# Performance work log

Measured on AMD Instinct MI355X. Metric: run time of the kernel, lower is better.

The kernel has to match this reference:

```python
import jax, jax.numpy as jnp
import numpy as np

B = 1024      # batch
H = 512       # n_hidden
F = 32        # lstm_features
CIN = 4       # input channels
K = 30        # conv kernel
STRIDE = 6
L = 924       # input length -> T = (924-30)//6+1 = 150
KD = 40       # deconv kernel
NSTEPS = 10   # lstm_future_out
DN = ('NCH', 'OIH', 'NCH')


def setup_inputs() -> dict:
    key = jax.random.key(0)
    ks = jax.random.split(key, 14)
    s = 0.05
    rn = lambda k, shape: jax.random.normal(k, shape, jnp.float32) * s
    return dict(
        x=jax.random.normal(ks[0], (B, CIN, L), jnp.float32),
        conv_w=rn(ks[1], (F, CIN, K)), conv_b=rn(ks[2], (F,)),
        Wih0=rn(ks[3], (4 * H, F)), Whh0=rn(ks[4], (4 * H, H)),
        bih0=rn(ks[5], (4 * H,)), bhh0=rn(ks[6], (4 * H,)),
        Wih1=rn(ks[7], (4 * H, H)), Whh1=rn(ks[8], (4 * H, H)),
        bih1=rn(ks[9], (4 * H,)), bhh1=rn(ks[10], (4 * H,)),
        dec_w=rn(ks[11], (F, H)), dec_b=rn(ks[12], (F,)),
        deconv_w=rn(ks[13], (F, 1, KD)),
    )


def _cell(x, h, c, Wih, Whh, b):
    # PyTorch LSTM gate order: i, f, g, o
    g = x @ Wih.T + h @ Whh.T + b
    i, f, gg, o = jnp.split(g, 4, axis=-1)
    c = jax.nn.sigmoid(f) * c + jax.nn.sigmoid(i) * jnp.tanh(gg)
    h = jax.nn.sigmoid(o) * jnp.tanh(c)
    return h, c


def _lstm_layer(seq, Wih, Whh, b):
    # seq: [T, B, in] -> ys: [T, B, H], final (h, c)
    n = seq.shape[1]
    h0 = jnp.zeros((n, H), seq.dtype)
    c0 = jnp.zeros((n, H), seq.dtype)
    def step(carry, x):
        h, c = _cell(x, carry[0], carry[1], Wih, Whh, b)
        return (h, c), h
    (hT, cT), ys = jax.lax.scan(step, (h0, c0), seq)
    return ys, hT, cT


def _forward(x, conv_w, conv_b, Wih0, Whh0, bih0, bhh0,
             Wih1, Whh1, bih1, bhh1, dec_w, dec_b, deconv_w):
    # encoder conv: [B,4,L] -> [B,F,T]
    z = jax.lax.conv_general_dilated(x, conv_w, (STRIDE,), [(0, 0)],
                                     dimension_numbers=DN) + conv_b[None, :, None]
    z = jax.nn.relu(z)
    seq = jnp.transpose(z, (2, 0, 1))  # [T, B, F]
    b0, b1 = bih0 + bhh0, bih1 + bhh1
    s0, h0, c0 = _lstm_layer(seq, Wih0, Whh0, b0)
    s1, h1, c1 = _lstm_layer(s0, Wih1, Whh1, b1)
    out = s1 @ dec_w.T + dec_b                 # [T, B, F]
    y0 = out[-1]                               # output[-2:-1] of encoder -> last decoded step
    def dec_step(carry, _):
        y, ha, ca, hb, cb = carry
        ha, ca = _cell(y, ha, ca, Wih0, Whh0, b0)
        hb, cb = _cell(ha, hb, cb, Wih1, Whh1, b1)
        y = hb @ dec_w.T + dec_b
        return (y, ha, ca, hb, cb), y
    _, fut = jax.lax.scan(dec_step, (y0, h0, c0, h1, c1), None, length=NSTEPS)
    fut = jnp.transpose(fut, (1, 2, 0))        # [B, F, 10]
    # ConvTranspose1d (stride=1, pad=0, no bias) == cross-correlation with
    # spatially flipped, channel-swapped kernel on input padded by KD-1.
    kt = jnp.transpose(jnp.flip(deconv_w, -1), (1, 0, 2))  # [1, F, KD]
    return jax.lax.conv_general_dilated(fut, kt, (1,), [(KD - 1, KD - 1)],
                                        dimension_numbers=DN)  # [B, 1, 49]


def reference(x, conv_w, conv_b, Wih0, Whh0, bih0, bhh0,
              Wih1, Whh1, bih1, bhh1, dec_w, dec_b, deconv_w):
    return _forward(x, conv_w, conv_b, Wih0, Whh0, bih0, bhh0,
                    Wih1, Whh1, bih1, bhh1, dec_w, dec_b, deconv_w)
```

## Files before the change

kernel.cpp:

```cpp
#include <hip/hip_runtime.h>
#include <hip/hip_bf16.h>

typedef __hip_bfloat16 bf16;
typedef __attribute__((ext_vector_type(8))) short short8;
typedef __attribute__((ext_vector_type(4))) float float4v;

#define B_    1024
#define H_    512
#define G4H   2048
#define F_    32
#define CIN_  4
#define K_    30
#define STRIDE_ 6
#define L_    924
#define T_    150
#define KD_   40
#define NSTEPS_ 10
#define BH    (B_ * H_)
#define STRF  16

__device__ __forceinline__ float sigmoidf_(float x) { return 1.f / (1.f + __expf(-x)); }
__device__ __forceinline__ float tanhf_(float x)    { return 1.f - 2.f / (__expf(2.f * x) + 1.f); }
__device__ __forceinline__ float b2f_(short s) {
    return __uint_as_float(((unsigned)(unsigned short)s) << 16);
}
__device__ __forceinline__ void stwt_(bf16* p, float v) {
    union { __hip_bfloat16 b; unsigned short u; } cv;
    cv.b = __float2bfloat16(v);
    __hip_atomic_store((unsigned short*)p, cv.u, __ATOMIC_RELAXED, __HIP_MEMORY_SCOPE_AGENT);
}

__global__ __launch_bounds__(256) void cvt_kernel(const float* __restrict__ src,
                                                  bf16* __restrict__ dst, int n) {
    int i = blockIdx.x * 256 + threadIdx.x;
    if (i < n) dst[i] = __float2bfloat16(src[i]);
}

__global__ void bias_kernel(const float* __restrict__ bih0, const float* __restrict__ bhh0,
                            const float* __restrict__ bih1, const float* __restrict__ bhh1,
                            float* __restrict__ b0, float* __restrict__ b1) {
    int i = blockIdx.x * 256 + threadIdx.x;
    if (i < G4H)      b0[i] = bih0[i] + bhh0[i];
    else if (i < 2*G4H) { int j = i - G4H; b1[j] = bih1[j] + bhh1[j]; }
}

__global__ __launch_bounds__(256) void conv_kernel(
    const float* __restrict__ x, const float* __restrict__ w,
    const float* __restrict__ cb, bf16* __restrict__ seq)
{
    __shared__ float w_lds[CIN_ * K_ * F_];
    __shared__ float x_lds[CIN_ * L_];
    int tid = threadIdx.x;
    int b = blockIdx.x;
    for (int i = tid; i < CIN_ * K_ * F_; i += 256) {
        int f = i & 31, r = i >> 5;
        w_lds[r * 32 + f] = w[f * (CIN_ * K_) + r];
    }
    const float* xb = x + (size_t)b * (CIN_ * L_);
    for (int i = tid; i < CIN_ * L_; i += 256)
        x_lds[i] = xb[i];
    __syncthreads();
    int f = tid & 31, tt = tid >> 5;
    float cbf = cb[f];
    for (int t0 = 0; t0 < T_; t0 += 8) {
        int t = t0 + tt;
        if (t < T_) {
            float acc = cbf;
            #pragma unroll
            for (int c = 0; c < CIN_; ++c) {
                const float* xr = x_lds + c * L_ + t * STRIDE_;
                const float* wr = w_lds + c * K_ * 32 + f;
                #pragma unroll
                for (int k = 0; k < K_; ++k)
                    acc += xr[k] * wr[k * 32];
            }
            acc = fmaxf(acc, 0.f);
            seq[(size_t)t * (B_ * F_) + b * F_ + f] = __float2bfloat16(acc);
        }
    }
}

__device__ __forceinline__ void wait2(const int* fa, int ta, const int* fb, int tb) {
    const int t = threadIdx.x;
    if (t < 64) {
        const int* p = nullptr; int tgt = 0;
        if (t < 32) { if (fa) { p = fa + t * STRF;        tgt = ta; } }
        else        { if (fb) { p = fb + (t - 32) * STRF; tgt = tb; } }
        for (;;) {
            int v = p ? __hip_atomic_load(p, __ATOMIC_RELAXED, __HIP_MEMORY_SCOPE_AGENT)
                      : 0x7fffffff;
            if (__all(v >= tgt)) break;
            __builtin_amdgcn_s_sleep(2);
        }
    }
    __syncthreads();
    __builtin_amdgcn_fence(__ATOMIC_ACQUIRE, "agent");
}

__device__ __forceinline__ void signal1(int* f, int val) {
    __syncthreads();
    if (threadIdx.x == 0) {
        __builtin_amdgcn_s_waitcnt(0);
        __hip_atomic_store(f, val, __ATOMIC_RELAXED, __HIP_MEMORY_SCOPE_AGENT);
    }
}

template<int P1KS, int XSTR>
__device__ __forceinline__ void layer_step(
    const bf16* __restrict__ X, const bf16* __restrict__ Hprev,
    const short8* __restrict__ WldsH, const short8* __restrict__ WldsI,
    const float* __restrict__ bias, float (&creg)[16], bf16* __restrict__ Hout,
    int m0, int j0, int wid, int lane)
{
    const int row16 = lane & 15;
    const int quad  = lane >> 4;
    const int mrow  = m0 + wid * 64 + row16;

    float4v acc[4][4];
    #pragma unroll
    for (int ms = 0; ms < 4; ++ms)
        #pragma unroll
        for (int g = 0; g < 4; ++g)
            acc[ms][g] = (float4v){0.f, 0.f, 0.f, 0.f};

    for (int ks = 0; ks < P1KS; ++ks) {
        short8 av[4];
        #pragma unroll
        for (int ms = 0; ms < 4; ++ms)
            av[ms] = *(const short8*)(X + (size_t)(mrow + ms * 16) * XSTR
                                      + ks * 32 + quad * 8);
        #pragma unroll
        for (int g = 0; g < 4; ++g) {
            short8 bfr = WldsI[(ks * 4 + g) * 64 + lane];
            #pragma unroll
            for (int ms = 0; ms < 4; ++ms)
                acc[ms][g] = __builtin_amdgcn_mfma_f32_16x16x32_bf16(av[ms], bfr, acc[ms][g], 0, 0, 0);
        }
    }

    for (int ks = 0; ks < 16; ++ks) {
        short8 av[4];
        #pragma unroll
        for (int ms = 0; ms < 4; ++ms)
            av[ms] = *(const short8*)(Hprev + (size_t)(mrow + ms * 16) * H_
                                      + ks * 32 + quad * 8);
        #pragma unroll
        for (int g = 0; g < 4; ++g) {
            short8 bfr = WldsH[(ks * 4 + g) * 64 + lane];
            #pragma unroll
            for (int ms = 0; ms < 4; ++ms)
                acc[ms][g] = __builtin_amdgcn_mfma_f32_16x16x32_bf16(av[ms], bfr, acc[ms][g], 0, 0, 0);
        }
    }

    const int j = j0 + row16;
    const float bi  = bias[j];
    const float bff = bias[H_ + j];
    const float bg  = bias[2 * H_ + j];
    const float bo  = bias[3 * H_ + j];
    #pragma unroll
    for (int ms = 0; ms < 4; ++ms) {
        #pragma unroll
        for (int r = 0; r < 4; ++r) {
            int brow = m0 + wid * 64 + ms * 16 + quad * 4 + r;
            float ig = sigmoidf_(acc[ms][0][r] + bi);
            float fg = sigmoidf_(acc[ms][1][r] + bff);
            float gg = tanhf_(acc[ms][2][r] + bg);
            float og = sigmoidf_(acc[ms][3][r] + bo);
            float cn = fg * creg[ms * 4 + r] + ig * gg;
            creg[ms * 4 + r] = cn;
            stwt_(Hout + (size_t)brow * H_ + j, og * tanhf_(cn));
        }
    }
}

struct PP {
    const bf16 *seq, *Wih0, *Whh0, *Wih1, *Whh1, *dwb;
    const float *b0, *b1, *dec_b;
    float *fut;
    bf16 *h0, *h1, *y;
    int *flags;
};

__global__ __launch_bounds__(256, 1) void lstm_persist(PP P) {
    __shared__ short8 WldsH[4096];
    __shared__ short8 WldsI[4096];

    const int bid   = blockIdx.x;
    const int gsw   = bid & 7;
    const bool isL0 = (gsw < 4);
    const int mg    = gsw & 3;
    const int jj    = bid >> 3;
    const int lb    = mg * 32 + jj;
    const int j0    = jj * 16;
    const int m0    = mg * 256;
    const int tid   = threadIdx.x;
    const int wid   = tid >> 6;
    const int lane  = tid & 63;

    {
        const bf16* Whh = isL0 ? P.Whh0 : P.Whh1;
        for (int i = 0; i < 16; ++i) {
            int s = tid + i * 256;
            int frag = s >> 6, ln = s & 63;
            int ks = frag >> 2, g = frag & 3;
            WldsH[s] = *(const short8*)(Whh + (size_t)(g * H_ + j0 + (ln & 15)) * H_
                                        + ks * 32 + (ln >> 4) * 8);
        }
        if (isL0) {
            if (tid < 256) {
                int frag = tid >> 6, ln = tid & 63;
                int g = frag & 3;
                WldsI[tid] = *(const short8*)(P.Wih0 + (size_t)(g * H_ + j0 + (ln & 15)) * F_
                                              + (ln >> 4) * 8);
            }
        } else {
            for (int i = 0; i < 16; ++i) {
                int s = tid + i * 256;
                int frag = s >> 6, ln = s & 63;
                int ks = frag >> 2, g = frag & 3;
                WldsI[s] = *(const short8*)(P.Wih1 + (size_t)(g * H_ + j0 + (ln & 15)) * H_
                                            + ks * 32 + (ln >> 4) * 8);
            }
        }
        __syncthreads();
    }

    float creg[16];
    #pragma unroll
    for (int i = 0; i < 16; ++i) creg[i] = 0.f;

    int* f0 = P.flags;
    int* f1 = P.flags + 128 * STRF;
    int* fy = P.flags + 256 * STRF;
    const int* f0g = f0 + mg * 32 * STRF;
    const int* f1g = f1 + mg * 32 * STRF;
    const int* fyg = fy + mg * 32 * STRF;

    if (isL0) {
        for (int t = 0; t < T_; ++t) {
            wait2(f0g, t, f1g, t - 2);
            layer_step<1, 32>(P.seq + (size_t)t * B_ * F_,
                              P.h0 + (size_t)((t + 2) % 3) * BH, WldsH, WldsI, P.b0,
                              creg, P.h0 + (size_t)(t % 3) * BH, m0, j0, wid, lane);
            signal1(f0 + lb * STRF, t + 1);
        }
        for (int s = 0; s <= NSTEPS_; ++s) {
            wait2(f1g, T_ + s, (s >= 1) ? f0g : nullptr, T_ + s);
            {
                int id = lb * 256 + tid;
                int br = id >> 5, f = id & 31;
                const short8* hv = (const short8*)(P.h1 + (size_t)((T_ - 1 + s) % 3) * BH
                                                   + (size_t)br * H_);
                const short8* wv = (const short8*)(P.dwb + (size_t)f * H_);
                float acc = P.dec_b[f];
                for (int i = 0; i < H_ / 8; ++i) {
                    short8 h8 = hv[i], w8 = wv[i];
                    #pragma unroll
                    for (int k = 0; k < 8; ++k)
                        acc += b2f_(h8[k]) * b2f_(w8[k]);
                }
                stwt_(P.y + id, acc);
                if (s >= 1)
                    P.fut[(size_t)br * (F_ * NSTEPS_) + f * NSTEPS_ + (s - 1)] = acc;
            }
            signal1(fy + lb * STRF, s + 1);
            if (s < NSTEPS_) {
                int t = T_ + s;
                wait2(f0g, t, f1g, t - 2);
                wait2(fyg, s + 1, nullptr, 0);
                layer_step<1, 32>(P.y,
                                  P.h0 + (size_t)((t + 2) % 3) * BH, WldsH, WldsI, P.b0,
                                  creg, P.h0 + (size_t)(t % 3) * BH, m0, j0, wid, lane);
                signal1(f0 + lb * STRF, t + 1);
            }
        }
    } else {
        for (int t = 0; t < T_ + NSTEPS_; ++t) {
            wait2(f0g, t + 1, f1g, t);
            layer_step<16, 512>(P.h0 + (size_t)(t % 3) * BH,
                                P.h1 + (size_t)((t + 2) % 3) * BH, WldsH, WldsI, P.b1,
                                creg, P.h1 + (size_t)(t % 3) * BH, m0, j0, wid, lane);
            signal1(f1 + lb * STRF, t + 1);
        }
    }
}

__global__ __launch_bounds__(256) void deconv_kernel(
    const float* __restrict__ fut, const float* __restrict__ dw,
    float* __restrict__ out)
{
    int idx = blockIdx.x * 256 + threadIdx.x;
    if (idx >= B_ * 49) return;
    int b = idx / 49, jj = idx % 49;
    int tlo = jj - (KD_ - 1); if (tlo < 0) tlo = 0;
    int thi = jj; if (thi > NSTEPS_ - 1) thi = NSTEPS_ - 1;
    float acc = 0.f;
    for (int f = 0; f < F_; ++f) {
        const float* fr = fut + (size_t)b * (F_ * NSTEPS_) + f * NSTEPS_;
        const float* wr = dw + f * KD_;
        for (int t = tlo; t <= thi; ++t)
            acc += fr[t] * wr[jj - t];
    }
    out[idx] = acc;
}

extern "C" void kernel_launch(void* const* d_in, const int* in_sizes, int n_in,
                              void* d_out, int out_size, void* d_ws, size_t ws_size,
                              hipStream_t stream) {
    const float* x       = (const float*)d_in[0];
    const float* conv_w  = (const float*)d_in[1];
    const float* conv_b  = (const float*)d_in[2];
    const float* Wih0f   = (const float*)d_in[3];
    const float* Whh0f   = (const float*)d_in[4];
    const float* bih0    = (const float*)d_in[5];
    const float* bhh0    = (const float*)d_in[6];
    const float* Wih1f   = (const float*)d_in[7];
    const float* Whh1f   = (const float*)d_in[8];
    const float* bih1    = (const float*)d_in[9];
    const float* bhh1    = (const float*)d_in[10];
    const float* dec_wf  = (const float*)d_in[11];
    const float* dec_b   = (const float*)d_in[12];
    const float* deconvw = (const float*)d_in[13];
    float* out = (float*)d_out;

    char* ws = (char*)d_ws;
    size_t off = 0;
    auto alloc = [&](size_t bytes) { char* p = ws + off; off = (off + bytes + 255) & ~(size_t)255; return p; };
    bf16*  seq   = (bf16*) alloc((size_t)T_ * B_ * F_ * 2);
    float* b0v   = (float*)alloc(G4H * 4);
    float* b1v   = (float*)alloc(G4H * 4);
    bf16*  h0    = (bf16*) alloc((size_t)3 * BH * 2);
    bf16*  h1    = (bf16*) alloc((size_t)3 * BH * 2);
    bf16*  y     = (bf16*) alloc((size_t)B_ * F_ * 2);
    float* fut   = (float*)alloc((size_t)B_ * F_ * NSTEPS_ * 4);
    bf16*  Wih0b = (bf16*) alloc((size_t)G4H * F_ * 2);
    bf16*  Whh0b = (bf16*) alloc((size_t)G4H * H_ * 2);
    bf16*  Wih1b = (bf16*) alloc((size_t)G4H * H_ * 2);
    bf16*  Whh1b = (bf16*) alloc((size_t)G4H * H_ * 2);
    bf16*  dec_wb= (bf16*) alloc((size_t)F_ * H_ * 2);
    int*   flags = (int*)  alloc(3 * 128 * STRF * 4);

    hipMemsetAsync(h0, 0, (size_t)3 * BH * 2, stream);
    hipMemsetAsync(h1, 0, (size_t)3 * BH * 2, stream);
    hipMemsetAsync(flags, 0, 3 * 128 * STRF * 4, stream);

    cvt_kernel<<<(G4H * F_ + 255) / 256, 256, 0, stream>>>(Wih0f, Wih0b, G4H * F_);
    cvt_kernel<<<(G4H * H_ + 255) / 256, 256, 0, stream>>>(Whh0f, Whh0b, G4H * H_);
    cvt_kernel<<<(G4H * H_ + 255) / 256, 256, 0, stream>>>(Wih1f, Wih1b, G4H * H_);
    cvt_kernel<<<(G4H * H_ + 255) / 256, 256, 0, stream>>>(Whh1f, Whh1b, G4H * H_);
    cvt_kernel<<<(F_ * H_ + 255) / 256, 256, 0, stream>>>(dec_wf, dec_wb, F_ * H_);

    bias_kernel<<<16, 256, 0, stream>>>(bih0, bhh0, bih1, bhh1, b0v, b1v);
    conv_kernel<<<B_, 256, 0, stream>>>(x, conv_w, conv_b, seq);

    PP P;
    P.seq = seq; P.Wih0 = Wih0b; P.Whh0 = Whh0b; P.Wih1 = Wih1b; P.Whh1 = Whh1b;
    P.dwb = dec_wb; P.b0 = b0v; P.b1 = b1v; P.dec_b = dec_b;
    P.fut = fut; P.h0 = h0; P.h1 = h1; P.y = y;
    P.flags = flags;

    void* args[] = { &P };
    hipError_t err = hipLaunchCooperativeKernel((const void*)lstm_persist,
                                                dim3(256), dim3(256), args, 0, stream);
    if (err != hipSuccess) {
        lstm_persist<<<256, 256, 0, stream>>>(P);
    }

    deconv_kernel<<<196, 256, 0, stream>>>(fut, deconvw, out);
}
```

Baseline: 4.870 ms.

## Split LSTM step waits so independent GEMM halves overlap flag polling

```diff
diff --git a/kernel.cpp b/kernel.cpp
--- a/kernel.cpp
+++ b/kernel.cpp
@@ -17,7 +17,6 @@
 #define KD_   40
 #define NSTEPS_ 10
 #define BH    (B_ * H_)
-#define STRF  16
 
 __device__ __forceinline__ float sigmoidf_(float x) { return 1.f / (1.f + __expf(-x)); }
 __device__ __forceinline__ float tanhf_(float x)    { return 1.f - 2.f / (__expf(2.f * x) + 1.f); }
@@ -80,21 +79,23 @@
     }
 }
 
-__device__ __forceinline__ void wait2(const int* fa, int ta, const int* fb, int tb) {
-    const int t = threadIdx.x;
-    if (t < 64) {
-        const int* p = nullptr; int tgt = 0;
-        if (t < 32) { if (fa) { p = fa + t * STRF;        tgt = ta; } }
-        else        { if (fb) { p = fb + (t - 32) * STRF; tgt = tb; } }
-        for (;;) {
-            int v = p ? __hip_atomic_load(p, __ATOMIC_RELAXED, __HIP_MEMORY_SCOPE_AGENT)
-                      : 0x7fffffff;
-            if (__all(v >= tgt)) break;
-            __builtin_amdgcn_s_sleep(2);
-        }
-    }
-    __syncthreads();
-    __builtin_amdgcn_fence(__ATOMIC_ACQUIRE, "agent");
+__device__ __forceinline__ void wait1(const int* fg, int tgt, bool inv) {
+    if (tgt > 0) {
+        if (threadIdx.x < 16) {
+            const long long* p = (const long long*)fg + threadIdx.x;
+            for (int n = 0; ; ++n) {
+                long long v = __hip_atomic_load(p, __ATOMIC_RELAXED, __HIP_MEMORY_SCOPE_AGENT);
+                int a = (int)v, b = (int)(v >> 32);
+                if (__all(a >= tgt && b >= tgt)) break;
+                if (n < 2) __builtin_amdgcn_s_sleep(2);
+                else       __builtin_amdgcn_s_sleep(32);
+            }
+        }
+        __syncthreads();
+        if (inv) __builtin_amdgcn_fence(__ATOMIC_ACQUIRE, "agent");
+    } else {
+        __syncthreads();
+    }
 }
 
 __device__ __forceinline__ void signal1(int* f, int val) {
@@ -105,25 +106,13 @@
     }
 }
 
-template<int P1KS, int XSTR>
-__device__ __forceinline__ void layer_step(
-    const bf16* __restrict__ X, const bf16* __restrict__ Hprev,
-    const short8* __restrict__ WldsH, const short8* __restrict__ WldsI,
-    const float* __restrict__ bias, float (&creg)[16], bf16* __restrict__ Hout,
-    int m0, int j0, int wid, int lane)
+#define MFMA_ __builtin_amdgcn_mfma_f32_16x16x32_bf16
+template<int NKS, int XSTR>
+__device__ __forceinline__ void gemm_acc(
+    const bf16* __restrict__ X, const short8* __restrict__ W,
+    float4v (&acc)[4][4], int mrow, int quad, int lane)
 {
-    const int row16 = lane & 15;
-    const int quad  = lane >> 4;
-    const int mrow  = m0 + wid * 64 + row16;
-
-    float4v acc[4][4];
-    #pragma unroll
-    for (int ms = 0; ms < 4; ++ms)
-        #pragma unroll
-        for (int g = 0; g < 4; ++g)
-            acc[ms][g] = (float4v){0.f, 0.f, 0.f, 0.f};
-
-    for (int ks = 0; ks < P1KS; ++ks) {
+    for (int ks = 0; ks < NKS; ++ks) {
         short8 av[4];
         #pragma unroll
         for (int ms = 0; ms < 4; ++ms)
@@ -131,28 +120,20 @@
                                       + ks * 32 + quad * 8);
         #pragma unroll
         for (int g = 0; g < 4; ++g) {
-            short8 bfr = WldsI[(ks * 4 + g) * 64 + lane];
+            short8 bfr = W[(ks * 4 + g) * 64 + lane];
             #pragma unroll
             for (int ms = 0; ms < 4; ++ms)
-                acc[ms][g] = __builtin_amdgcn_mfma_f32_16x16x32_bf16(av[ms], bfr, acc[ms][g], 0, 0, 0);
-        }
-    }
-
-    for (int ks = 0; ks < 16; ++ks) {
-        short8 av[4];
-        #pragma unroll
-        for (int ms = 0; ms < 4; ++ms)
-            av[ms] = *(const short8*)(Hprev + (size_t)(mrow + ms * 16) * H_
-                                      + ks * 32 + quad * 8);
-        #pragma unroll
-        for (int g = 0; g < 4; ++g) {
-            short8 bfr = WldsH[(ks * 4 + g) * 64 + lane];
-            #pragma unroll
-            for (int ms = 0; ms < 4; ++ms)
-                acc[ms][g] = __builtin_amdgcn_mfma_f32_16x16x32_bf16(av[ms], bfr, acc[ms][g], 0, 0, 0);
-        }
-    }
-
+                acc[ms][g] = MFMA_(av[ms], bfr, acc[ms][g], 0, 0, 0);
+        }
+    }
+}
+
+__device__ __forceinline__ void epilogue_(
+    float4v (&acc)[4][4], float (&creg)[16], const float* __restrict__ bias,
+    bf16* __restrict__ Hout, int m0, int j0, int wid, int lane)
+{
+    const int row16 = lane & 15;
+    const int quad  = lane >> 4;
     const int j = j0 + row16;
     const float bi  = bias[j];
     const float bff = bias[H_ + j];
@@ -197,6 +178,8 @@
     const int tid   = threadIdx.x;
     const int wid   = tid >> 6;
     const int lane  = tid & 63;
+    const int quad  = lane >> 4;
+    const int mrow  = m0 + wid * 64 + (lane & 15);
 
     {
         const bf16* Whh = isL0 ? P.Whh0 : P.Whh1;
@@ -231,57 +214,77 @@
     for (int i = 0; i < 16; ++i) creg[i] = 0.f;
 
     int* f0 = P.flags;
-    int* f1 = P.flags + 128 * STRF;
-    int* fy = P.flags + 256 * STRF;
-    const int* f0g = f0 + mg * 32 * STRF;
-    const int* f1g = f1 + mg * 32 * STRF;
-    const int* fyg = fy + mg * 32 * STRF;
+    int* f1 = P.flags + 128;
+    int* fy = P.flags + 256;
+    const int* f0g = f0 + mg * 32;
+    const int* f1g = f1 + mg * 32;
+    const int* fyg = fy + mg * 32;
+
+    float4v acc[4][4];
 
     if (isL0) {
         for (int t = 0; t < T_; ++t) {
-            wait2(f0g, t, f1g, t - 2);
-            layer_step<1, 32>(P.seq + (size_t)t * B_ * F_,
-                              P.h0 + (size_t)((t + 2) % 3) * BH, WldsH, WldsI, P.b0,
-                              creg, P.h0 + (size_t)(t % 3) * BH, m0, j0, wid, lane);
-            signal1(f0 + lb * STRF, t + 1);
+            wait1(f1g, t - 2, false);
+            #pragma unroll
+            for (int ms = 0; ms < 4; ++ms)
+                #pragma unroll
+                for (int g = 0; g < 4; ++g) acc[ms][g] = (float4v){0.f,0.f,0.f,0.f};
+            gemm_acc<1, 32>(P.seq + (size_t)t * B_ * F_, WldsI, acc, mrow, quad, lane);
+            wait1(f0g, t, true);
+            gemm_acc<16, 512>(P.h0 + (size_t)((t + 2) % 3) * BH, WldsH, acc, mrow, quad, lane);
+            epilogue_(acc, creg, P.b0, P.h0 + (size_t)(t % 3) * BH, m0, j0, wid, lane);
+            signal1(f0 + lb, t + 1);
         }
         for (int s = 0; s <= NSTEPS_; ++s) {
-            wait2(f1g, T_ + s, (s >= 1) ? f0g : nullptr, T_ + s);
+            wait1(f1g, T_ + s, true);
+            float yacc;
+            int id = lb * 256 + tid;
             {
-                int id = lb * 256 + tid;
                 int br = id >> 5, f = id & 31;
                 const short8* hv = (const short8*)(P.h1 + (size_t)((T_ - 1 + s) % 3) * BH
                                                    + (size_t)br * H_);
                 const short8* wv = (const short8*)(P.dwb + (size_t)f * H_);
-                float acc = P.dec_b[f];
+                yacc = P.dec_b[f];
                 for (int i = 0; i < H_ / 8; ++i) {
                     short8 h8 = hv[i], w8 = wv[i];
                     #pragma unroll
                     for (int k = 0; k < 8; ++k)
-                        acc += b2f_(h8[k]) * b2f_(w8[k]);
+                        yacc += b2f_(h8[k]) * b2f_(w8[k]);
                 }
-                stwt_(P.y + id, acc);
-                if (s >= 1)
-                    P.fut[(size_t)br * (F_ * NSTEPS_) + f * NSTEPS_ + (s - 1)] = acc;
-            }
-            signal1(fy + lb * STRF, s + 1);
+            }
+            if (s >= 1) wait1(f0g, T_ + s, false);
+            stwt_(P.y + id, yacc);
+            if (s >= 1) {
+                int br = id >> 5, f = id & 31;
+                P.fut[(size_t)br * (F_ * NSTEPS_) + f * NSTEPS_ + (s - 1)] = yacc;
+            }
+            signal1(fy + lb, s + 1);
             if (s < NSTEPS_) {
                 int t = T_ + s;
-                wait2(f0g, t, f1g, t - 2);
-                wait2(fyg, s + 1, nullptr, 0);
-                layer_step<1, 32>(P.y,
-                                  P.h0 + (size_t)((t + 2) % 3) * BH, WldsH, WldsI, P.b0,
-                                  creg, P.h0 + (size_t)(t % 3) * BH, m0, j0, wid, lane);
-                signal1(f0 + lb * STRF, t + 1);
+                wait1(fyg, s + 1, true);
+                #pragma unroll
+                for (int ms = 0; ms < 4; ++ms)
+                    #pragma unroll
+                    for (int g = 0; g < 4; ++g) acc[ms][g] = (float4v){0.f,0.f,0.f,0.f};
+                gemm_acc<1, 32>(P.y, WldsI, acc, mrow, quad, lane);
+                wait1(f0g, t, true);
+                gemm_acc<16, 512>(P.h0 + (size_t)((t + 2) % 3) * BH, WldsH, acc, mrow, quad, lane);
+                epilogue_(acc, creg, P.b0, P.h0 + (size_t)(t % 3) * BH, m0, j0, wid, lane);
+                signal1(f0 + lb, t + 1);
             }
         }
     } else {
         for (int t = 0; t < T_ + NSTEPS_; ++t) {
-            wait2(f0g, t + 1, f1g, t);
-            layer_step<16, 512>(P.h0 + (size_t)(t % 3) * BH,
-                                P.h1 + (size_t)((t + 2) % 3) * BH, WldsH, WldsI, P.b1,
-                                creg, P.h1 + (size_t)(t % 3) * BH, m0, j0, wid, lane);
-            signal1(f1 + lb * STRF, t + 1);
+            wait1(f1g, t, true);
+            #pragma unroll
+            for (int ms = 0; ms < 4; ++ms)
+                #pragma unroll
+                for (int g = 0; g < 4; ++g) acc[ms][g] = (float4v){0.f,0.f,0.f,0.f};
+            gemm_acc<16, 512>(P.h1 + (size_t)((t + 2) % 3) * BH, WldsH, acc, mrow, quad, lane);
+            wait1(f0g, t + 1, true);
+            gemm_acc<16, 512>(P.h0 + (size_t)(t % 3) * BH, WldsI, acc, mrow, quad, lane);
+            epilogue_(acc, creg, P.b1, P.h1 + (size_t)(t % 3) * BH, m0, j0, wid, lane);
+            signal1(f1 + lb, t + 1);
         }
     }
 }
@@ -339,11 +342,11 @@
     bf16*  Wih1b = (bf16*) alloc((size_t)G4H * H_ * 2);
     bf16*  Whh1b = (bf16*) alloc((size_t)G4H * H_ * 2);
     bf16*  dec_wb= (bf16*) alloc((size_t)F_ * H_ * 2);
-    int*   flags = (int*)  alloc(3 * 128 * STRF * 4);
+    int*   flags = (int*)  alloc(384 * 4);
 
     hipMemsetAsync(h0, 0, (size_t)3 * BH * 2, stream);
     hipMemsetAsync(h1, 0, (size_t)3 * BH * 2, stream);
-    hipMemsetAsync(flags, 0, 3 * 128 * STRF * 4, stream);
+    hipMemsetAsync(flags, 0, 384 * 4, stream);
 
     cvt_kernel<<<(G4H * F_ + 255) / 256, 256, 0, stream>>>(Wih0f, Wih0b, G4H * F_);
     cvt_kernel<<<(G4H * H_ + 255) / 256, 256, 0, stream>>>(Whh0f, Whh0b, G4H * H_);
```

New measurement: 5.901 ms. +21.2%, slower.
